# Kernel optimization log

Hardware: AMD Instinct MI355X
Metric: run time of the kernel (lower is better)

## Reference

```python
import jax, jax.numpy as jnp
import numpy as np

N, E, G = 100000, 300000, 4096
ND, ED, H, ZI, ZS, NE, L = 64, 16, 256, 128, 128, 8, 3
LAMBDA_GRL = 1.0


def setup_inputs() -> dict:
    key = jax.random.key(0)
    ks = iter(jax.random.split(key, 64))
    def nrm(shape, scale=0.05):
        return jax.random.normal(next(ks), shape, jnp.float32) * scale
    inp = {
        'x': jax.random.normal(next(ks), (N, ND), jnp.float32),
        'edge_index': jax.random.randint(next(ks), (2, E), 0, N),
        'edge_attr': jax.random.normal(next(ks), (E, ED), jnp.float32),
        'batch': jnp.sort(jax.random.randint(next(ks), (N,), 0, G)),
        'node_W': nrm((ND, H)), 'node_b': nrm((H,)),
        'conv_eps': jnp.zeros((L,), jnp.float32),
        'edge_W': nrm((L, ED, H)), 'edge_b': nrm((L, H)),
        'mlp_W1': nrm((L, H, H)), 'mlp_b1': nrm((L, H)),
        'mlp_W2': nrm((L, H, H)), 'mlp_b2': nrm((L, H)),
        'gn_w': jnp.ones((L, H), jnp.float32), 'gn_b': jnp.zeros((L, H), jnp.float32),
        'gn_ms': jnp.ones((L, H), jnp.float32),
        'finv_W1': nrm((H, ZI)), 'finv_b1': nrm((ZI,)),
        'finv_W2': nrm((ZI, ZI)), 'finv_b2': nrm((ZI,)),
        'fspu_W1': nrm((H, ZS)), 'fspu_b1': nrm((ZS,)),
        'fspu_W2': nrm((ZS, ZS)), 'fspu_b2': nrm((ZS,)),
        'pred_W1': nrm((ZI, ZI)), 'pred_b1': nrm((ZI,)),
        'pred_W2': nrm((ZI, 1)), 'pred_b2': nrm((1,)),
        'adv_W1': nrm((ZI, ZI)), 'adv_b1': nrm((ZI,)),
        'adv_W2': nrm((ZI, NE)), 'adv_b2': nrm((NE,)),
    }
    return inp


def _mlp2(h, W1, b1, W2, b2):
    return jax.nn.relu(h @ W1 + b1) @ W2 + b2


def reference(x, edge_index, edge_attr, batch, node_W, node_b, conv_eps,
              edge_W, edge_b, mlp_W1, mlp_b1, mlp_W2, mlp_b2,
              gn_w, gn_b, gn_ms,
              finv_W1, finv_b1, finv_W2, finv_b2,
              fspu_W1, fspu_b1, fspu_W2, fspu_b2,
              pred_W1, pred_b1, pred_W2, pred_b2,
              adv_W1, adv_b1, adv_W2, adv_b2):
    src, dst = edge_index[0], edge_index[1]
    cnt = jax.ops.segment_sum(jnp.ones((N, 1), jnp.float32), batch, num_segments=G)
    cnt = jnp.maximum(cnt, 1.0)
    h = x @ node_W + node_b  # [N,H]
    for l in range(L):
        # GINEConv: sum_j relu(x_j + lin(e_ij))
        e = edge_attr @ edge_W[l] + edge_b[l]            # [E,H]
        m = jax.nn.relu(h[src] + e)                      # [E,H]
        agg = jax.ops.segment_sum(m, dst, num_segments=N)
        h = _mlp2((1.0 + conv_eps[l]) * h + agg, mlp_W1[l], mlp_b1[l], mlp_W2[l], mlp_b2[l])
        # GraphNorm
        mean = jax.ops.segment_sum(h, batch, num_segments=G) / cnt  # [G,H]
        out = h - gn_ms[l] * mean[batch]
        var = jax.ops.segment_sum(out * out, batch, num_segments=G) / cnt
        h = out * jax.lax.rsqrt(var[batch] + 1e-5) * gn_w[l] + gn_b[l]
        h = jax.nn.relu(h)  # dropout is identity at eval
    hg = jax.ops.segment_sum(h, batch, num_segments=G) / cnt  # global_mean_pool [G,H]
    z_inv = _mlp2(hg, finv_W1, finv_b1, finv_W2, finv_b2)
    z_spu = _mlp2(hg, fspu_W1, fspu_b1, fspu_W2, fspu_b2)
    yhat = _mlp2(z_inv, pred_W1, pred_b1, pred_W2, pred_b2)[:, 0]
    # gradient reversal: identity fwd, -lambda on bwd
    grl = jax.lax.stop_gradient(z_inv) * (1.0 + LAMBDA_GRL) - LAMBDA_GRL * z_inv
    envhat = _mlp2(grl, adv_W1, adv_b1, adv_W2, adv_b2)
    return (hg, z_inv, z_spu, yhat, envhat)
```

## Files before the change

kernel.cpp:

```cpp
#include <hip/hip_runtime.h>
#include <hip/hip_bf16.h>

typedef __bf16 bf16_t;
typedef __bf16 bf16x8 __attribute__((ext_vector_type(8)));
typedef __bf16 bf16x4 __attribute__((ext_vector_type(4)));
typedef float  f32x4  __attribute__((ext_vector_type(4)));

static constexpr int N_NODES = 100000;
static constexpr int N_EDGES = 300000;
static constexpr int N_GRAPH = 4096;
static constexpr int H  = 256;
static constexpr int ND = 64;
static constexpr int ZIC = 128;
static constexpr int NE = 8;
static constexpr int SCAN_B = 1024;

__device__ __forceinline__ int clampi(int v, int lo, int hi) {
  return v < lo ? lo : (v > hi ? hi : v);
}

__device__ __forceinline__ void dma16(const bf16_t* g, bf16_t* lds_base) {
  __builtin_amdgcn_global_load_lds(
      (const __attribute__((address_space(1))) void*)g,
      (__attribute__((address_space(3))) void*)lds_base, 16, 0, 0);
}

__global__ void compute_starts_kernel(const int* __restrict__ batch,
                                      int* __restrict__ starts,
                                      int* __restrict__ counts,
                                      int* __restrict__ cursor, int N, int G) {
  int i = blockIdx.x * blockDim.x + threadIdx.x;
  if (i >= N) return;
  counts[i] = 0;
  cursor[i] = 0;
  int b = clampi(batch[i], 0, G - 1);
  if (i == 0) {
    for (int g = 0; g <= b; ++g) starts[g] = 0;
  } else {
    int p = clampi(batch[i - 1], 0, G - 1);
    for (int g = p + 1; g <= b; ++g) starts[g] = i;
  }
  if (i == N - 1) {
    for (int g = b + 1; g <= G; ++g) starts[g] = N;
  }
}

__global__ void count_deg_kernel(const int* __restrict__ dst, int* __restrict__ counts, int E, int N) {
  int e = blockIdx.x * blockDim.x + threadIdx.x;
  if (e < E) atomicAdd(&counts[clampi(dst[e], 0, N - 1)], 1);
}

__global__ __launch_bounds__(SCAN_B) void scan1_kernel(const int* __restrict__ counts,
                                                       int* __restrict__ offs,
                                                       int* __restrict__ bsum, int N) {
  __shared__ int tmp[SCAN_B];
  int i = blockIdx.x * SCAN_B + threadIdx.x;
  int v = (i < N) ? counts[i] : 0;
  tmp[threadIdx.x] = v;
  __syncthreads();
  for (int d = 1; d < SCAN_B; d <<= 1) {
    int t = (threadIdx.x >= d) ? tmp[threadIdx.x - d] : 0;
    __syncthreads();
    tmp[threadIdx.x] += t;
    __syncthreads();
  }
  if (i < N) offs[i + 1] = tmp[threadIdx.x];
  if (threadIdx.x == SCAN_B - 1) bsum[blockIdx.x] = tmp[SCAN_B - 1];
  if (i == 0) offs[0] = 0;
}

__global__ void scan2_kernel(int* __restrict__ bsum, int nblk) {
  if (blockIdx.x == 0 && threadIdx.x == 0) {
    int run = 0;
    for (int b = 0; b < nblk; ++b) { int v = bsum[b]; bsum[b] = run; run += v; }
  }
}

__global__ __launch_bounds__(SCAN_B) void scan3_kernel(int* __restrict__ offs,
                                                       const int* __restrict__ bsum, int N) {
  int i = blockIdx.x * SCAN_B + threadIdx.x;
  if (i < N) offs[i + 1] += bsum[blockIdx.x];
}

__global__ void fill_scatter_kernel(const int* __restrict__ src, const int* __restrict__ dst,
                                    const float* __restrict__ eattr,
                                    const int* __restrict__ offs, int* __restrict__ cursor,
                                    int* __restrict__ src_srt, bf16_t* __restrict__ eat16,
                                    int E, int N) {
  int e = blockIdx.x * blockDim.x + threadIdx.x;
  if (e >= E) return;
  int d = clampi(dst[e], 0, N - 1);
  int pos = offs[d] + atomicAdd(&cursor[d], 1);
  if ((unsigned)pos >= (unsigned)E) return;
  int s = src[e];
  src_srt[pos] = ((unsigned)s < (unsigned)N_NODES) ? s : 0;
  const float* ea = eattr + (size_t)e * 16;
  union { bf16_t b[16]; uint4 u[2]; } pk;
#pragma unroll
  for (int k = 0; k < 16; ++k) pk.b[k] = (bf16_t)ea[k];
  uint4* dst16 = (uint4*)(eat16 + ((size_t)pos << 4));
  dst16[0] = pk.u[0];
  dst16[1] = pk.u[1];
}

__global__ void build_ewt16_kernel(const float* __restrict__ edge_W,
                                   bf16_t* __restrict__ ewt) {
  int idx = blockIdx.x * blockDim.x + threadIdx.x;
  if (idx >= 3 * 256 * 16) return;
  int l = idx / (256 * 16);
  int rem = idx - l * 256 * 16;
  int n = rem >> 4, k = rem & 15;
  ewt[idx] = (bf16_t)edge_W[(size_t)l * 16 * 256 + k * 256 + n];
}

__global__ void transpose_kernel(const float* __restrict__ W,
                                 bf16_t* __restrict__ Wt, int K, int Nc,
                                 size_t srcStride, size_t dstStride) {
  __shared__ float tile[32][33];
  const float* Wz = W + (size_t)blockIdx.z * srcStride;
  bf16_t* Wtz = Wt + (size_t)blockIdx.z * dstStride;
  int n0 = blockIdx.x * 32, k0 = blockIdx.y * 32;
  int tx = threadIdx.x, ty = threadIdx.y;
  for (int i = ty; i < 32; i += 8)
    tile[i][tx] = Wz[(size_t)(k0 + i) * Nc + n0 + tx];
  __syncthreads();
  for (int i = ty; i < 32; i += 8)
    Wtz[(size_t)(n0 + i) * K + k0 + tx] = (bf16_t)tile[tx][i];
}

__device__ __forceinline__ void load8_to_lds(const bf16_t* p, bool valid, uint4* dst) {
  uint4 v = make_uint4(0u, 0u, 0u, 0u);
  if (valid) v = *(const uint4*)p;
  *dst = v;
}
__device__ __forceinline__ void load8_to_lds(const float* p, bool valid, uint4* dst) {
  float4 f0 = make_float4(0.f, 0.f, 0.f, 0.f), f1 = f0;
  if (valid) { f0 = *(const float4*)p; f1 = *(const float4*)(p + 4); }
  union { bf16_t b[8]; uint4 u; } pk;
  pk.b[0] = (bf16_t)f0.x; pk.b[1] = (bf16_t)f0.y;
  pk.b[2] = (bf16_t)f0.z; pk.b[3] = (bf16_t)f0.w;
  pk.b[4] = (bf16_t)f1.x; pk.b[5] = (bf16_t)f1.y;
  pk.b[6] = (bf16_t)f1.z; pk.b[7] = (bf16_t)f1.w;
  *dst = pk.u;
}

template<int K, bool RELU, bool OUTF32, typename TIN>
__global__ __launch_bounds__(256) void gemm128_kernel(
    const TIN* __restrict__ U, const bf16_t* __restrict__ Wt,
    const float* __restrict__ bias, void* __restrict__ Out, int M, int Nc) {
  constexpr int LDT = 72;
  __shared__ bf16_t Ut[128 * LDT];
  __shared__ bf16_t Wl[128 * LDT];
  const int m0 = blockIdx.x * 128;
  const int n0 = blockIdx.y * 128;
  const int t = threadIdx.x;
  const int lane = t & 63;
  const int wave = t >> 6;
  const int wm = (wave >> 1) * 64;
  const int wn = (wave & 1) * 64;
  const int srow = t >> 1;
  const int sk = (t & 1) * 32;
  const int lr = lane & 15;
  const int lq = lane >> 4;
  const bool aok = (m0 + srow) < M;
  f32x4 acc[4][4] = {};

  for (int k0 = 0; k0 < K; k0 += 64) {
    const TIN* up = U + (size_t)(m0 + srow) * K + k0 + sk;
    const bf16_t* wp = Wt + (size_t)(n0 + srow) * K + k0 + sk;
#pragma unroll
    for (int q = 0; q < 4; ++q) {
      load8_to_lds(up + q * 8, aok, (uint4*)&Ut[srow * LDT + sk + q * 8]);
      load8_to_lds(wp + q * 8, true, (uint4*)&Wl[srow * LDT + sk + q * 8]);
    }
    __syncthreads();
#pragma unroll
    for (int s = 0; s < 2; ++s) {
      bf16x8 a[4], b[4];
#pragma unroll
      for (int mt = 0; mt < 4; ++mt)
        a[mt] = *(const bf16x8*)(&Ut[(wm + mt * 16 + lr) * LDT + s * 32 + lq * 8]);
#pragma unroll
      for (int nt = 0; nt < 4; ++nt)
        b[nt] = *(const bf16x8*)(&Wl[(wn + nt * 16 + lr) * LDT + s * 32 + lq * 8]);
#pragma unroll
      for (int mt = 0; mt < 4; ++mt)
#pragma unroll
        for (int nt = 0; nt < 4; ++nt)
          acc[mt][nt] = __builtin_amdgcn_mfma_f32_16x16x32_bf16(
              a[mt], b[nt], acc[mt][nt], 0, 0, 0);
    }
    __syncthreads();
  }

#pragma unroll
  for (int mt = 0; mt < 4; ++mt)
#pragma unroll
    for (int nt = 0; nt < 4; ++nt) {
      int col = n0 + wn + nt * 16 + lr;
      float bcol = bias[col];
#pragma unroll
      for (int r = 0; r < 4; ++r) {
        int row = m0 + wm + mt * 16 + lq * 4 + r;
        if (row < M) {
          float vv = acc[mt][nt][r] + bcol;
          if (RELU) vv = vv > 0.f ? vv : 0.f;
          if (OUTF32) ((float*)Out)[(size_t)row * Nc + col] = vv;
          else        ((bf16_t*)Out)[(size_t)row * Nc + col] = (bf16_t)vv;
        }
      }
    }
}

template<int K, bool RELU, bool OUTF32, typename TIN>
__global__ __launch_bounds__(256) void gemm64x2_kernel(
    const TIN* __restrict__ U0, const bf16_t* __restrict__ Wt0,
    const float* __restrict__ b0, void* __restrict__ O0,
    const TIN* __restrict__ U1, const bf16_t* __restrict__ Wt1,
    const float* __restrict__ b1, void* __restrict__ O1, int M, int Nc) {
  constexpr int LDT = 72;
  __shared__ bf16_t Ut[64 * LDT];
  __shared__ bf16_t Wl[64 * LDT];
  const TIN*    U    = blockIdx.z ? U1 : U0;
  const bf16_t* Wt   = blockIdx.z ? Wt1 : Wt0;
  const float*  bias = blockIdx.z ? b1 : b0;
  void*         Out  = blockIdx.z ? O1 : O0;
  const int m0 = blockIdx.x * 64;
  const int n0 = blockIdx.y * 64;
  const int t = threadIdx.x;
  const int lane = t & 63;
  const int wave = t >> 6;
  const int wm = (wave >> 1) * 32;
  const int wn = (wave & 1) * 32;
  const int srow = t >> 2;
  const int sk = (t & 3) * 8;
  const int lr = lane & 15;
  const int lq = lane >> 4;
  const bool aok = (m0 + srow) < M;
  f32x4 acc[2][2] = {};

  for (int k0 = 0; k0 < K; k0 += 64) {
    const TIN* up = U + (size_t)(m0 + srow) * K + k0 + sk;
    const bf16_t* wp = Wt + (size_t)(n0 + srow) * K + k0 + sk;
    load8_to_lds(up,      aok, (uint4*)&Ut[srow * LDT + sk]);
    load8_to_lds(up + 32, aok, (uint4*)&Ut[srow * LDT + sk + 32]);
    load8_to_lds(wp,      true, (uint4*)&Wl[srow * LDT + sk]);
    load8_to_lds(wp + 32, true, (uint4*)&Wl[srow * LDT + sk + 32]);
    __syncthreads();
#pragma unroll
    for (int s = 0; s < 2; ++s) {
      bf16x8 a[2], b[2];
#pragma unroll
      for (int mt = 0; mt < 2; ++mt)
        a[mt] = *(const bf16x8*)(&Ut[(wm + mt * 16 + lr) * LDT + s * 32 + lq * 8]);
#pragma unroll
      for (int nt = 0; nt < 2; ++nt)
        b[nt] = *(const bf16x8*)(&Wl[(wn + nt * 16 + lr) * LDT + s * 32 + lq * 8]);
#pragma unroll
      for (int mt = 0; mt < 2; ++mt)
#pragma unroll
        for (int nt = 0; nt < 2; ++nt)
          acc[mt][nt] = __builtin_amdgcn_mfma_f32_16x16x32_bf16(
              a[mt], b[nt], acc[mt][nt], 0, 0, 0);
    }
    __syncthreads();
  }

#pragma unroll
  for (int mt = 0; mt < 2; ++mt)
#pragma unroll
    for (int nt = 0; nt < 2; ++nt) {
      int col = n0 + wn + nt * 16 + lr;
      float bcol = bias[col];
#pragma unroll
      for (int r = 0; r < 4; ++r) {
        int row = m0 + wm + mt * 16 + lq * 4 + r;
        if (row < M) {
          float vv = acc[mt][nt][r] + bcol;
          if (RELU) vv = vv > 0.f ? vv : 0.f;
          if (OUTF32) ((float*)Out)[(size_t)row * Nc + col] = vv;
          else        ((bf16_t*)Out)[(size_t)row * Nc + col] = (bf16_t)vv;
        }
      }
    }
}

template<int K, bool RELU>
__global__ __launch_bounds__(512) void gemm256_dma_kernel(
    const bf16_t* __restrict__ U, const bf16_t* __restrict__ Wt,
    const float* __restrict__ bias, bf16_t* __restrict__ Out, int M) {
  __shared__ bf16_t Ut[128 * 64];
  __shared__ bf16_t Wl[256 * 64];
  const int t = threadIdx.x;
  const int lane = t & 63;
  const int wave = t >> 6;
  const int m0 = blockIdx.x * 128;
  const int wm = (wave >> 2) * 64;
  const int wn = (wave & 3) * 64;
  const int lr = lane & 15;
  const int lq = lane >> 4;
  const int subrow = lane >> 3;
  const int lchunk = (lane & 7) ^ subrow;
  f32x4 acc[4][4] = {};

  for (int k0 = 0; k0 < K; k0 += 64) {
#pragma unroll
    for (int c = 0; c < 2; ++c) {
      int urow = m0 + c * 64 + wave * 8 + subrow;
      if (urow >= M) urow = M - 1;
      dma16(U + (size_t)urow * K + k0 + lchunk * 8, &Ut[(c * 64 + wave * 8) * 64]);
    }
#pragma unroll
    for (int c = 0; c < 4; ++c) {
      int wrow = c * 64 + wave * 8 + subrow;
      dma16(Wt + (size_t)wrow * K + k0 + lchunk * 8, &Wl[(c * 64 + wave * 8) * 64]);
    }
    __syncthreads();
#pragma unroll
    for (int s = 0; s < 2; ++s) {
      bf16x8 a[4], b[4];
#pragma unroll
      for (int mt = 0; mt < 4; ++mt)
        a[mt] = *(const bf16x8*)(&Ut[(wm + mt * 16 + lr) * 64 + (((s * 4 + lq) ^ (lr & 7)) << 3)]);
#pragma unroll
      for (int nt = 0; nt < 4; ++nt)
        b[nt] = *(const bf16x8*)(&Wl[(wn + nt * 16 + lr) * 64 + (((s * 4 + lq) ^ (lr & 7)) << 3)]);
#pragma unroll
      for (int mt = 0; mt < 4; ++mt)
#pragma unroll
        for (int nt = 0; nt < 4; ++nt)
          acc[mt][nt] = __builtin_amdgcn_mfma_f32_16x16x32_bf16(
              a[mt], b[nt], acc[mt][nt], 0, 0, 0);
    }
    __syncthreads();
  }

#pragma unroll
  for (int mt = 0; mt < 4; ++mt)
#pragma unroll
    for (int nt = 0; nt < 4; ++nt) {
      int col = wn + nt * 16 + lr;
      float bcol = bias[col];
#pragma unroll
      for (int r = 0; r < 4; ++r) {
        int row = m0 + wm + mt * 16 + lq * 4 + r;
        if (row < M) {
          float vv = acc[mt][nt][r] + bcol;
          if (RELU) vv = vv > 0.f ? vv : 0.f;
          Out[(size_t)row * H + col] = (bf16_t)vv;
        }
      }
    }
}

__global__ __launch_bounds__(256) void gine_gather_mfma_kernel(
    const bf16_t* __restrict__ h, const bf16_t* __restrict__ eat16,
    const int* __restrict__ src_sorted, const int* __restrict__ offs,
    const bf16_t* __restrict__ ewt, const float* __restrict__ eb,
    const float* __restrict__ eps_p, bf16_t* __restrict__ u) {
  constexpr int HP = H + 8;
  __shared__ bf16_t slin[2][16 * HP];
  const int t = threadIdx.x;
  const int wave = t >> 6;
  const int lane = t & 63;
  const int lr = lane & 15;
  const int lq = lane >> 4;
  const int lane4 = lane * 4;
  const int n0 = blockIdx.x * 4;
  const int nodeN = n0 + wave;

  bf16x4 hs = *(const bf16x4*)(h + (size_t)nodeN * H + lane4);

  bf16x8 bfrag[4];
#pragma unroll
  for (int nt = 0; nt < 4; ++nt) {
    bf16x8 bv = {};
    if (lq < 2)
      bv = *(const bf16x8*)(ewt + ((wave * 64 + nt * 16 + lr) << 4) + (lq << 3));
    bfrag[nt] = bv;
  }
  float ebv[4];
#pragma unroll
  for (int i = 0; i < 4; ++i) ebv[i] = eb[lane4 + i];

  int bs = offs[n0], be = offs[n0 + 4];
  bs = clampi(bs, 0, N_EDGES);
  be = clampi(be, bs, N_EDGES);
  int ns = offs[nodeN], ne = offs[nodeN + 1];
  ns = clampi(ns, bs, be);
  ne = clampi(ne, ns, be);

  float acc[4] = {0.f, 0.f, 0.f, 0.f};
  int parity = 0;

  for (int cb = bs; cb < be; cb += 16, parity ^= 1) {
    int arow = cb + lr;
    if (arow >= N_EDGES) arow = N_EDGES - 1;
    bf16x8 afrag = {};
    if (lq < 2)
      afrag = *(const bf16x8*)(eat16 + ((size_t)arow << 4) + (lq << 3));

    int j0 = ns > cb ? ns : cb;
    int j1 = ne < cb + 16 ? ne : cb + 16;
    int sidx[4];
    bf16x4 hv[4];
    if (j0 < j1) {
#pragma unroll
      for (int q = 0; q < 4; ++q) {
        int jj = j0 + q; if (jj > j1 - 1) jj = j1 - 1;
        sidx[q] = src_sorted[jj];
      }
    }

    f32x4 c[4];
#pragma unroll
    for (int nt = 0; nt < 4; ++nt) {
      f32x4 z = {};
      c[nt] = __builtin_amdgcn_mfma_f32_16x16x32_bf16(afrag, bfrag[nt], z, 0, 0, 0);
    }
#pragma unroll
    for (int nt = 0; nt < 4; ++nt)
#pragma unroll
      for (int r = 0; r < 4; ++r)
        slin[parity][(lq * 4 + r) * HP + wave * 64 + nt * 16 + lr] = (bf16_t)c[nt][r];

    if (j0 < j1) {
#pragma unroll
      for (int q = 0; q < 4; ++q)
        hv[q] = *(const bf16x4*)(h + (size_t)sidx[q] * H + lane4);
    }

    __syncthreads();

    for (int jb = j0; jb < j1; jb += 4) {
      if (jb != j0) {
#pragma unroll
        for (int q = 0; q < 4; ++q) {
          int jj = jb + q; if (jj > j1 - 1) jj = j1 - 1;
          sidx[q] = src_sorted[jj];
        }
#pragma unroll
        for (int q = 0; q < 4; ++q)
          hv[q] = *(const bf16x4*)(h + (size_t)sidx[q] * H + lane4);
      }
#pragma unroll
      for (int q = 0; q < 4; ++q) {
        if (jb + q < j1) {
          bf16x4 lv = *(const bf16x4*)(&slin[parity][(jb + q - cb) * HP + lane4]);
#pragma unroll
          for (int i = 0; i < 4; ++i)
            acc[i] += fmaxf((float)hv[q][i] + (float)lv[i] + ebv[i], 0.f);
        }
      }
    }
  }

  const float sc = 1.0f + eps_p[0];
  union { bf16x4 v; uint2 b; } o;
#pragma unroll
  for (int i = 0; i < 4; ++i) o.v[i] = (bf16_t)(sc * (float)hs[i] + acc[i]);
  *(uint2*)(u + (size_t)nodeN * H + lane4) = o.b;
}

__global__ __launch_bounds__(256) void graphnorm_kernel(
    const bf16_t* __restrict__ v, bf16_t* __restrict__ hout,
    const int* __restrict__ starts,
    const float* __restrict__ w, const float* __restrict__ b,
    const float* __restrict__ ms, float* __restrict__ hg) {
  constexpr int RS = 9;
  constexpr int PS = 13;
  __shared__ float red[4 * 64 * RS];
  __shared__ float prm[64 * PS];
  const int g = blockIdx.x;
  const int t = threadIdx.x;
  const int lane = t & 63;
  const int wave = t >> 6;
  const int c0 = lane * 4;
  int s = starts[g], e = starts[g + 1];
  s = clampi(s, 0, N_NODES);
  e = clampi(e, s, N_NODES);
  const float cnt = (float)((e - s) > 1 ? (e - s) : 1);

  float sx[4] = {0.f, 0.f, 0.f, 0.f}, sxx[4] = {0.f, 0.f, 0.f, 0.f};
  {
    int i = s + wave;
    for (; i + 4 < e; i += 8) {
      bf16x4 x0 = *(const bf16x4*)(v + (size_t)i * H + c0);
      bf16x4 x1 = *(const bf16x4*)(v + (size_t)(i + 4) * H + c0);
#pragma unroll
      for (int j = 0; j < 4; ++j) {
        float f0 = (float)x0[j], f1 = (float)x1[j];
        sx[j] += f0 + f1; sxx[j] += f0 * f0 + f1 * f1;
      }
    }
    if (i < e) {
      bf16x4 x0 = *(const bf16x4*)(v + (size_t)i * H + c0);
#pragma unroll
      for (int j = 0; j < 4; ++j) {
        float f0 = (float)x0[j];
        sx[j] += f0; sxx[j] += f0 * f0;
      }
    }
  }
  float* myred = &red[(wave * 64 + lane) * RS];
#pragma unroll
  for (int j = 0; j < 4; ++j) { myred[j] = sx[j]; myred[4 + j] = sxx[j]; }
  __syncthreads();

  if (wave == 0) {
#pragma unroll
    for (int j = 0; j < 4; ++j) {
      float fsx = red[lane * RS + j] + red[(64 + lane) * RS + j] +
                  red[(128 + lane) * RS + j] + red[(192 + lane) * RS + j];
      float fsxx = red[lane * RS + 4 + j] + red[(64 + lane) * RS + 4 + j] +
                   red[(128 + lane) * RS + 4 + j] + red[(192 + lane) * RS + 4 + j];
      float mean = fsx / cnt;
      float sub = ms[c0 + j] * mean;
      float var = fsxx / cnt - 2.f * sub * mean + sub * sub;
      var = fmaxf(var, 0.f);
      prm[lane * PS + j] = sub;
      prm[lane * PS + 4 + j] = rsqrtf(var + 1e-5f) * w[c0 + j];
      prm[lane * PS + 8 + j] = b[c0 + j];
    }
  }
  __syncthreads();
  float sub[4], inv[4], bb[4];
#pragma unroll
  for (int j = 0; j < 4; ++j) {
    sub[j] = prm[lane * PS + j];
    inv[j] = prm[lane * PS + 4 + j];
    bb[j] = prm[lane * PS + 8 + j];
  }

  float psum[4] = {0.f, 0.f, 0.f, 0.f};
  {
    int i = s + wave;
    for (; i + 4 < e; i += 8) {
      bf16x4 x0 = *(const bf16x4*)(v + (size_t)i * H + c0);
      bf16x4 x1 = *(const bf16x4*)(v + (size_t)(i + 4) * H + c0);
      union { bf16x4 o; uint2 u; } p0, p1;
#pragma unroll
      for (int j = 0; j < 4; ++j) {
        float o0 = ((float)x0[j] - sub[j]) * inv[j] + bb[j];
        float o1 = ((float)x1[j] - sub[j]) * inv[j] + bb[j];
        o0 = o0 > 0.f ? o0 : 0.f;
        o1 = o1 > 0.f ? o1 : 0.f;
        psum[j] += o0 + o1;
        p0.o[j] = (bf16_t)o0; p1.o[j] = (bf16_t)o1;
      }
      *(uint2*)(hout + (size_t)i * H + c0) = p0.u;
      *(uint2*)(hout + (size_t)(i + 4) * H + c0) = p1.u;
    }
    if (i < e) {
      bf16x4 x0 = *(const bf16x4*)(v + (size_t)i * H + c0);
      union { bf16x4 o; uint2 u; } p0;
#pragma unroll
      for (int j = 0; j < 4; ++j) {
        float o0 = ((float)x0[j] - sub[j]) * inv[j] + bb[j];
        o0 = o0 > 0.f ? o0 : 0.f;
        psum[j] += o0;
        p0.o[j] = (bf16_t)o0;
      }
      *(uint2*)(hout + (size_t)i * H + c0) = p0.u;
    }
  }

  if (hg) {
#pragma unroll
    for (int j = 0; j < 4; ++j) myred[j] = psum[j];
    __syncthreads();
    if (wave == 0) {
#pragma unroll
      for (int j = 0; j < 4; ++j) {
        float p = red[lane * RS + j] + red[(64 + lane) * RS + j] +
                  red[(128 + lane) * RS + j] + red[(192 + lane) * RS + j];
        hg[(size_t)g * H + c0 + j] = p / cnt;
      }
    }
  }
}

__global__ void head_out2_kernel(const bf16_t* __restrict__ In1, const float* __restrict__ W1,
                                 const float* __restrict__ b1, float* __restrict__ O1,
                                 const bf16_t* __restrict__ In2, const float* __restrict__ W2,
                                 const float* __restrict__ b2, float* __restrict__ O2,
                                 int M) {
  int idx = blockIdx.x * blockDim.x + threadIdx.x;
  if (idx < M) {
    float acc = b1[0];
    const bf16_t* in = In1 + (size_t)idx * ZIC;
    for (int k = 0; k < ZIC; ++k) acc += (float)in[k] * W1[k];
    O1[idx] = acc;
  } else {
    int j = idx - M;
    if (j >= M * NE) return;
    int r = j >> 3, n = j & 7;
    float acc = b2[n];
    const bf16_t* in = In2 + (size_t)r * ZIC;
    for (int k = 0; k < ZIC; ++k) acc += (float)in[k] * W2[(size_t)k * NE + n];
    O2[j] = acc;
  }
}

extern "C" void kernel_launch(void* const* d_in, const int* in_sizes, int n_in,
                              void* d_out, int out_size, void* d_ws, size_t ws_size,
                              hipStream_t stream) {
  (void)in_sizes; (void)n_in; (void)out_size; (void)ws_size;
  const float* x        = (const float*)d_in[0];
  const int*   eidx     = (const int*)d_in[1];
  const float* eattr    = (const float*)d_in[2];
  const int*   batch    = (const int*)d_in[3];
  const float* node_W   = (const float*)d_in[4];
  const float* node_b   = (const float*)d_in[5];
  const float* conv_eps = (const float*)d_in[6];
  const float* edge_W   = (const float*)d_in[7];
  const float* edge_b   = (const float*)d_in[8];
  const float* mlp_W1   = (const float*)d_in[9];
  const float* mlp_b1   = (const float*)d_in[10];
  const float* mlp_W2   = (const float*)d_in[11];
  const float* mlp_b2   = (const float*)d_in[12];
  const float* gn_w     = (const float*)d_in[13];
  const float* gn_b     = (const float*)d_in[14];
  const float* gn_ms    = (const float*)d_in[15];
  const float* finv_W1  = (const float*)d_in[16];
  const float* finv_b1  = (const float*)d_in[17];
  const float* finv_W2  = (const float*)d_in[18];
  const float* finv_b2  = (const float*)d_in[19];
  const float* fspu_W1  = (const float*)d_in[20];
  const float* fspu_b1  = (const float*)d_in[21];
  const float* fspu_W2  = (const float*)d_in[22];
  const float* fspu_b2  = (const float*)d_in[23];
  const float* pred_W1  = (const float*)d_in[24];
  const float* pred_b1  = (const float*)d_in[25];
  const float* pred_W2  = (const float*)d_in[26];
  const float* pred_b2  = (const float*)d_in[27];
  const float* adv_W1   = (const float*)d_in[28];
  const float* adv_b1   = (const float*)d_in[29];
  const float* adv_W2   = (const float*)d_in[30];
  const float* adv_b2   = (const float*)d_in[31];
  float* out = (float*)d_out;

  float* out_hg = out;
  float* out_zi = out + (size_t)N_GRAPH * H;
  float* out_zs = out_zi + (size_t)N_GRAPH * ZIC;
  float* out_yh = out_zs + (size_t)N_GRAPH * ZIC;
  float* out_ev = out_yh + N_GRAPH;

  char* wp = (char*)d_ws;
  auto alloc = [&](size_t bytes) { char* p = wp; wp += (bytes + 255) & ~(size_t)255; return p; };
  bf16_t* A        = (bf16_t*)alloc((size_t)N_NODES * H * 2);
  bf16_t* B        = (bf16_t*)alloc((size_t)N_NODES * H * 2);
  bf16_t* Wt       = (bf16_t*)alloc((size_t)(H * ND + 6 * H * H) * 2);
  bf16_t* WtH      = (bf16_t*)alloc((size_t)(2 * ZIC * H + 4 * ZIC * ZIC) * 2);
  bf16_t* ewt16    = (bf16_t*)alloc((size_t)3 * 256 * 16 * 2);
  bf16_t* eat16    = (bf16_t*)alloc((size_t)N_EDGES * 16 * 2);
  int*    starts   = (int*)alloc((size_t)(N_GRAPH + 1) * 4);
  int*    counts   = (int*)alloc((size_t)N_NODES * 4);
  int*    cursor   = (int*)alloc((size_t)N_NODES * 4);
  int*    offs     = (int*)alloc((size_t)(N_NODES + 1) * 4);
  int*    bsum     = (int*)alloc((size_t)SCAN_B * 4);
  int*    src_srt  = (int*)alloc((size_t)N_EDGES * 4);
  bf16_t* tmp1     = (bf16_t*)alloc((size_t)N_GRAPH * ZIC * 2);
  bf16_t* tmp2     = (bf16_t*)alloc((size_t)N_GRAPH * ZIC * 2);

  const int* srcp = eidx;
  const int* dstp = eidx + N_EDGES;
  const int nscan = (N_NODES + SCAN_B - 1) / SCAN_B;

  compute_starts_kernel<<<(N_NODES + 255) / 256, 256, 0, stream>>>(
      batch, starts, counts, cursor, N_NODES, N_GRAPH);
  count_deg_kernel<<<(N_EDGES + 255) / 256, 256, 0, stream>>>(dstp, counts, N_EDGES, N_NODES);
  scan1_kernel<<<nscan, SCAN_B, 0, stream>>>(counts, offs, bsum, N_NODES);
  scan2_kernel<<<1, 64, 0, stream>>>(bsum, nscan);
  scan3_kernel<<<nscan, SCAN_B, 0, stream>>>(offs, bsum, N_NODES);
  fill_scatter_kernel<<<(N_EDGES + 255) / 256, 256, 0, stream>>>(
      srcp, dstp, eattr, offs, cursor, src_srt, eat16, N_EDGES, N_NODES);
  build_ewt16_kernel<<<(3 * 256 * 16 + 255) / 256, 256, 0, stream>>>(edge_W, ewt16);

  bf16_t* WtN = Wt;
  bf16_t* Wt1base = Wt + H * ND;
  bf16_t* Wt2base = Wt + H * ND + (size_t)H * H;
  auto Wt1l = [&](int l) { return Wt1base + (size_t)(2 * l) * H * H; };
  auto Wt2l = [&](int l) { return Wt2base + (size_t)(2 * l) * H * H; };
  transpose_kernel<<<dim3(H / 32, ND / 32, 1), dim3(32, 8), 0, stream>>>(node_W, WtN, ND, H, 0, 0);
  transpose_kernel<<<dim3(H / 32, H / 32, 3), dim3(32, 8), 0, stream>>>(
      mlp_W1, Wt1base, H, H, (size_t)H * H, (size_t)2 * H * H);
  transpose_kernel<<<dim3(H / 32, H / 32, 3), dim3(32, 8), 0, stream>>>(
      mlp_W2, Wt2base, H, H, (size_t)H * H, (size_t)2 * H * H);

  bf16_t* fT1 = WtH;
  bf16_t* fT2 = fT1 + ZIC * H;
  bf16_t* sT1 = fT2 + ZIC * ZIC;
  bf16_t* sT2 = sT1 + ZIC * H;
  bf16_t* pT1 = sT2 + ZIC * ZIC;
  bf16_t* aT1 = pT1 + ZIC * ZIC;
  transpose_kernel<<<dim3(ZIC / 32, H / 32, 1), dim3(32, 8), 0, stream>>>(finv_W1, fT1, H, ZIC, 0, 0);
  transpose_kernel<<<dim3(ZIC / 32, ZIC / 32, 1), dim3(32, 8), 0, stream>>>(finv_W2, fT2, ZIC, ZIC, 0, 0);
  transpose_kernel<<<dim3(ZIC / 32, H / 32, 1), dim3(32, 8), 0, stream>>>(fspu_W1, sT1, H, ZIC, 0, 0);
  transpose_kernel<<<dim3(ZIC / 32, ZIC / 32, 1), dim3(32, 8), 0, stream>>>(fspu_W2, sT2, ZIC, ZIC, 0, 0);
  transpose_kernel<<<dim3(ZIC / 32, ZIC / 32, 1), dim3(32, 8), 0, stream>>>(pred_W1, pT1, ZIC, ZIC, 0, 0);
  transpose_kernel<<<dim3(ZIC / 32, ZIC / 32, 1), dim3(32, 8), 0, stream>>>(adv_W1, aT1, ZIC, ZIC, 0, 0);

  dim3 ggrid((N_NODES + 127) / 128, H / 128);
  gemm128_kernel<ND, false, false><<<ggrid, 256, 0, stream>>>(x, WtN, node_b, A, N_NODES, H);

  const int mblocks = (N_NODES + 127) / 128;
  for (int l = 0; l < 3; ++l) {
    gine_gather_mfma_kernel<<<N_NODES / 4, 256, 0, stream>>>(
        A, eat16, src_srt, offs, ewt16 + (size_t)l * 256 * 16,
        edge_b + l * H, conv_eps + l, B);
    gemm256_dma_kernel<H, true ><<<mblocks, 512, 0, stream>>>(B, Wt1l(l), mlp_b1 + l * H, A, N_NODES);
    gemm256_dma_kernel<H, false><<<mblocks, 512, 0, stream>>>(A, Wt2l(l), mlp_b2 + l * H, B, N_NODES);
    graphnorm_kernel<<<N_GRAPH, 256, 0, stream>>>(B, A, starts, gn_w + l * H, gn_b + l * H,
                                                  gn_ms + l * H, (l == 2) ? out_hg : nullptr);
  }

  dim3 hgrid2(N_GRAPH / 64, ZIC / 64, 2);
  gemm64x2_kernel<H, true, false, float><<<hgrid2, 256, 0, stream>>>(
      out_hg, fT1, finv_b1, tmp1, out_hg, sT1, fspu_b1, tmp2, N_GRAPH, ZIC);
  gemm64x2_kernel<ZIC, false, true, bf16_t><<<hgrid2, 256, 0, stream>>>(
      tmp1, fT2, finv_b2, out_zi, tmp2, sT2, fspu_b2, out_zs, N_GRAPH, ZIC);
  gemm64x2_kernel<ZIC, true, false, float><<<hgrid2, 256, 0, stream>>>(
      out_zi, pT1, pred_b1, tmp1, out_zi, aT1, adv_b1, tmp2, N_GRAPH, ZIC);
  head_out2_kernel<<<(N_GRAPH * (1 + NE) + 255) / 256, 256, 0, stream>>>(
      tmp1, pred_W2, pred_b2, out_yh, tmp2, adv_W2, adv_b2, out_ev, N_GRAPH);
}
```

Measured before the change: 729.0 us.

## Fuse the two MLP GEMMs per layer, keeping the hidden activation in LDS

Replaces the two separate 256-wide GEMM launches of each GIN MLP with one kernel. It computes relu(U·W1+b1) into a swizzled 128x256 LDS tile and then multiplies that tile by W2. This removes the global write and re-read of the intermediate activation and one launch per layer. The W1 transpose gains a channel permutation so each lane's accumulator columns pack contiguously into LDS. Weight fragments are now loaded straight from global memory (L2) instead of being staged in LDS. The larger LDS footprint may also reduce occupancy.

```diff
diff --git a/kernel.cpp b/kernel.cpp
--- a/kernel.cpp
+++ b/kernel.cpp
@@ -126,6 +126,24 @@
   __syncthreads();
   for (int i = ty; i < 32; i += 8)
     Wtz[(size_t)(n0 + i) * K + k0 + tx] = (bf16_t)tile[tx][i];
+}
+
+__global__ void transpose_perm_kernel(const float* __restrict__ W,
+                                      bf16_t* __restrict__ Wt, int K,
+                                      size_t srcStride, size_t dstStride) {
+  __shared__ float tile[32][33];
+  const float* Wz = W + (size_t)blockIdx.z * srcStride;
+  bf16_t* Wtz = Wt + (size_t)blockIdx.z * dstStride;
+  int n0 = blockIdx.x * 32, k0 = blockIdx.y * 32;
+  int tx = threadIdx.x, ty = threadIdx.y;
+  for (int i = ty; i < 32; i += 8)
+    tile[i][tx] = Wz[(size_t)(k0 + i) * 256 + n0 + tx];
+  __syncthreads();
+  for (int i = ty; i < 32; i += 8) {
+    int n = n0 + i;
+    int s = ((n & 15) << 4) | (n >> 4);
+    Wtz[(size_t)s * K + k0 + tx] = (bf16_t)tile[tx][i];
+  }
 }
 
 __device__ __forceinline__ void load8_to_lds(const bf16_t* p, bool valid, uint4* dst) {
@@ -285,12 +303,13 @@
     }
 }
 
-template<int K, bool RELU>
-__global__ __launch_bounds__(512) void gemm256_dma_kernel(
-    const bf16_t* __restrict__ U, const bf16_t* __restrict__ Wt,
-    const float* __restrict__ bias, bf16_t* __restrict__ Out, int M) {
+template<int K>
+__global__ __launch_bounds__(512, 4) void mlp_fused_kernel(
+    const bf16_t* __restrict__ U, const bf16_t* __restrict__ W1p,
+    const float* __restrict__ b1, const bf16_t* __restrict__ W2t,
+    const float* __restrict__ b2, bf16_t* __restrict__ Out, int M) {
+  __shared__ bf16_t T[128 * 256];
   __shared__ bf16_t Ut[128 * 64];
-  __shared__ bf16_t Wl[256 * 64];
   const int t = threadIdx.x;
   const int lane = t & 63;
   const int wave = t >> 6;
@@ -310,21 +329,16 @@
       if (urow >= M) urow = M - 1;
       dma16(U + (size_t)urow * K + k0 + lchunk * 8, &Ut[(c * 64 + wave * 8) * 64]);
     }
-#pragma unroll
-    for (int c = 0; c < 4; ++c) {
-      int wrow = c * 64 + wave * 8 + subrow;
-      dma16(Wt + (size_t)wrow * K + k0 + lchunk * 8, &Wl[(c * 64 + wave * 8) * 64]);
-    }
     __syncthreads();
 #pragma unroll
     for (int s = 0; s < 2; ++s) {
       bf16x8 a[4], b[4];
 #pragma unroll
+      for (int nt = 0; nt < 4; ++nt)
+        b[nt] = *(const bf16x8*)(W1p + (size_t)(wn + nt * 16 + lr) * K + k0 + s * 32 + lq * 8);
+#pragma unroll
       for (int mt = 0; mt < 4; ++mt)
         a[mt] = *(const bf16x8*)(&Ut[(wm + mt * 16 + lr) * 64 + (((s * 4 + lq) ^ (lr & 7)) << 3)]);
-#pragma unroll
-      for (int nt = 0; nt < 4; ++nt)
-        b[nt] = *(const bf16x8*)(&Wl[(wn + nt * 16 + lr) * 64 + (((s * 4 + lq) ^ (lr & 7)) << 3)]);
 #pragma unroll
       for (int mt = 0; mt < 4; ++mt)
 #pragma unroll
@@ -335,18 +349,64 @@
     __syncthreads();
   }
 
+  {
+    const int ch0 = lr * 16 + (wave & 3) * 4;
+    float b1v[4];
+#pragma unroll
+    for (int nt = 0; nt < 4; ++nt) b1v[nt] = b1[ch0 + nt];
+#pragma unroll
+    for (int mt = 0; mt < 4; ++mt)
+#pragma unroll
+      for (int r = 0; r < 4; ++r) {
+        int row = wm + mt * 16 + lq * 4 + r;
+        union { bf16_t b[4]; uint2 u2; } pk;
+#pragma unroll
+        for (int nt = 0; nt < 4; ++nt) {
+          float vv = acc[mt][nt][r] + b1v[nt];
+          pk.b[nt] = (bf16_t)(vv > 0.f ? vv : 0.f);
+        }
+        *(uint2*)((char*)T + (row << 9) + ((ch0 * 2) ^ ((row & 7) << 4))) = pk.u2;
+      }
+  }
+  __syncthreads();
+
+#pragma unroll
+  for (int mt = 0; mt < 4; ++mt)
+#pragma unroll
+    for (int nt = 0; nt < 4; ++nt) {
+      f32x4 z = {};
+      acc[mt][nt] = z;
+    }
+  for (int k2 = 0; k2 < K; k2 += 32) {
+    bf16x8 a[4], b[4];
+#pragma unroll
+    for (int nt = 0; nt < 4; ++nt)
+      b[nt] = *(const bf16x8*)(W2t + (size_t)(wn + nt * 16 + lr) * K + k2 + lq * 8);
+#pragma unroll
+    for (int mt = 0; mt < 4; ++mt) {
+      int row = wm + mt * 16 + lr;
+      a[mt] = *(const bf16x8*)((const char*)T + (row << 9) +
+                               (((k2 + lq * 8) * 2) ^ ((row & 7) << 4)));
+    }
+#pragma unroll
+    for (int mt = 0; mt < 4; ++mt)
+#pragma unroll
+      for (int nt = 0; nt < 4; ++nt)
+        acc[mt][nt] = __builtin_amdgcn_mfma_f32_16x16x32_bf16(
+            a[mt], b[nt], acc[mt][nt], 0, 0, 0);
+  }
+
 #pragma unroll
   for (int mt = 0; mt < 4; ++mt)
 #pragma unroll
     for (int nt = 0; nt < 4; ++nt) {
       int col = wn + nt * 16 + lr;
-      float bcol = bias[col];
+      float bcol = b2[col];
 #pragma unroll
       for (int r = 0; r < 4; ++r) {
         int row = m0 + wm + mt * 16 + lq * 4 + r;
         if (row < M) {
           float vv = acc[mt][nt][r] + bcol;
-          if (RELU) vv = vv > 0.f ? vv : 0.f;
           Out[(size_t)row * H + col] = (bf16_t)vv;
         }
       }
@@ -683,8 +743,8 @@
   auto Wt1l = [&](int l) { return Wt1base + (size_t)(2 * l) * H * H; };
   auto Wt2l = [&](int l) { return Wt2base + (size_t)(2 * l) * H * H; };
   transpose_kernel<<<dim3(H / 32, ND / 32, 1), dim3(32, 8), 0, stream>>>(node_W, WtN, ND, H, 0, 0);
-  transpose_kernel<<<dim3(H / 32, H / 32, 3), dim3(32, 8), 0, stream>>>(
-      mlp_W1, Wt1base, H, H, (size_t)H * H, (size_t)2 * H * H);
+  transpose_perm_kernel<<<dim3(H / 32, H / 32, 3), dim3(32, 8), 0, stream>>>(
+      mlp_W1, Wt1base, H, (size_t)H * H, (size_t)2 * H * H);
   transpose_kernel<<<dim3(H / 32, H / 32, 3), dim3(32, 8), 0, stream>>>(
       mlp_W2, Wt2base, H, H, (size_t)H * H, (size_t)2 * H * H);
 
@@ -709,8 +769,8 @@
     gine_gather_mfma_kernel<<<N_NODES / 4, 256, 0, stream>>>(
         A, eat16, src_srt, offs, ewt16 + (size_t)l * 256 * 16,
         edge_b + l * H, conv_eps + l, B);
-    gemm256_dma_kernel<H, true ><<<mblocks, 512, 0, stream>>>(B, Wt1l(l), mlp_b1 + l * H, A, N_NODES);
-    gemm256_dma_kernel<H, false><<<mblocks, 512, 0, stream>>>(A, Wt2l(l), mlp_b2 + l * H, B, N_NODES);
+    mlp_fused_kernel<H><<<mblocks, 512, 0, stream>>>(
+        B, Wt1l(l), mlp_b1 + l * H, Wt2l(l), mlp_b2 + l * H, B, N_NODES);
     graphnorm_kernel<<<N_GRAPH, 256, 0, stream>>>(B, A, starts, gn_w + l * H, gn_b + l * H,
                                                   gn_ms + l * H, (l == 2) ? out_hg : nullptr);
   }
```

Measured after the change: 755.6 us. +3.6%, slower.

## Fuse all prediction-head MLP layers into one kernel with LDS intermediates

Applied to the files above, without the earlier changes.

Replaces the three two-way GEMM launches and the final output kernel with a single kernel. Each block processes 64 graphs through the finv/fspu MLPs, the pred/adv first layers and the final projections, keeping intermediates in shared memory. This removes launch overhead and global round-trips of temporary buffers, but uses only 64 blocks and reads weight operands directly from global memory.

```diff
diff --git a/kernel.cpp b/kernel.cpp
--- a/kernel.cpp
+++ b/kernel.cpp
@@ -212,79 +212,6 @@
     }
 }
 
-template<int K, bool RELU, bool OUTF32, typename TIN>
-__global__ __launch_bounds__(256) void gemm64x2_kernel(
-    const TIN* __restrict__ U0, const bf16_t* __restrict__ Wt0,
-    const float* __restrict__ b0, void* __restrict__ O0,
-    const TIN* __restrict__ U1, const bf16_t* __restrict__ Wt1,
-    const float* __restrict__ b1, void* __restrict__ O1, int M, int Nc) {
-  constexpr int LDT = 72;
-  __shared__ bf16_t Ut[64 * LDT];
-  __shared__ bf16_t Wl[64 * LDT];
-  const TIN*    U    = blockIdx.z ? U1 : U0;
-  const bf16_t* Wt   = blockIdx.z ? Wt1 : Wt0;
-  const float*  bias = blockIdx.z ? b1 : b0;
-  void*         Out  = blockIdx.z ? O1 : O0;
-  const int m0 = blockIdx.x * 64;
-  const int n0 = blockIdx.y * 64;
-  const int t = threadIdx.x;
-  const int lane = t & 63;
-  const int wave = t >> 6;
-  const int wm = (wave >> 1) * 32;
-  const int wn = (wave & 1) * 32;
-  const int srow = t >> 2;
-  const int sk = (t & 3) * 8;
-  const int lr = lane & 15;
-  const int lq = lane >> 4;
-  const bool aok = (m0 + srow) < M;
-  f32x4 acc[2][2] = {};
-
-  for (int k0 = 0; k0 < K; k0 += 64) {
-    const TIN* up = U + (size_t)(m0 + srow) * K + k0 + sk;
-    const bf16_t* wp = Wt + (size_t)(n0 + srow) * K + k0 + sk;
-    load8_to_lds(up,      aok, (uint4*)&Ut[srow * LDT + sk]);
-    load8_to_lds(up + 32, aok, (uint4*)&Ut[srow * LDT + sk + 32]);
-    load8_to_lds(wp,      true, (uint4*)&Wl[srow * LDT + sk]);
-    load8_to_lds(wp + 32, true, (uint4*)&Wl[srow * LDT + sk + 32]);
-    __syncthreads();
-#pragma unroll
-    for (int s = 0; s < 2; ++s) {
-      bf16x8 a[2], b[2];
-#pragma unroll
-      for (int mt = 0; mt < 2; ++mt)
-        a[mt] = *(const bf16x8*)(&Ut[(wm + mt * 16 + lr) * LDT + s * 32 + lq * 8]);
-#pragma unroll
-      for (int nt = 0; nt < 2; ++nt)
-        b[nt] = *(const bf16x8*)(&Wl[(wn + nt * 16 + lr) * LDT + s * 32 + lq * 8]);
-#pragma unroll
-      for (int mt = 0; mt < 2; ++mt)
-#pragma unroll
-        for (int nt = 0; nt < 2; ++nt)
-          acc[mt][nt] = __builtin_amdgcn_mfma_f32_16x16x32_bf16(
-              a[mt], b[nt], acc[mt][nt], 0, 0, 0);
-    }
-    __syncthreads();
-  }
-
-#pragma unroll
-  for (int mt = 0; mt < 2; ++mt)
-#pragma unroll
-    for (int nt = 0; nt < 2; ++nt) {
-      int col = n0 + wn + nt * 16 + lr;
-      float bcol = bias[col];
-#pragma unroll
-      for (int r = 0; r < 4; ++r) {
-        int row = m0 + wm + mt * 16 + lq * 4 + r;
-        if (row < M) {
-          float vv = acc[mt][nt][r] + bcol;
-          if (RELU) vv = vv > 0.f ? vv : 0.f;
-          if (OUTF32) ((float*)Out)[(size_t)row * Nc + col] = vv;
-          else        ((bf16_t*)Out)[(size_t)row * Nc + col] = (bf16_t)vv;
-        }
-      }
-    }
-}
-
 template<int K, bool RELU>
 __global__ __launch_bounds__(512) void gemm256_dma_kernel(
     const bf16_t* __restrict__ U, const bf16_t* __restrict__ Wt,
@@ -580,25 +507,178 @@
   }
 }
 
-__global__ void head_out2_kernel(const bf16_t* __restrict__ In1, const float* __restrict__ W1,
-                                 const float* __restrict__ b1, float* __restrict__ O1,
-                                 const bf16_t* __restrict__ In2, const float* __restrict__ W2,
-                                 const float* __restrict__ b2, float* __restrict__ O2,
-                                 int M) {
-  int idx = blockIdx.x * blockDim.x + threadIdx.x;
-  if (idx < M) {
-    float acc = b1[0];
-    const bf16_t* in = In1 + (size_t)idx * ZIC;
-    for (int k = 0; k < ZIC; ++k) acc += (float)in[k] * W1[k];
-    O1[idx] = acc;
-  } else {
-    int j = idx - M;
-    if (j >= M * NE) return;
+__global__ __launch_bounds__(256) void heads_fused_kernel(
+    const float* __restrict__ hg,
+    const bf16_t* __restrict__ fT1, const float* __restrict__ fb1,
+    const bf16_t* __restrict__ fT2, const float* __restrict__ fb2,
+    const bf16_t* __restrict__ sT1, const float* __restrict__ sb1,
+    const bf16_t* __restrict__ sT2, const float* __restrict__ sb2,
+    const bf16_t* __restrict__ pT1, const float* __restrict__ pb1,
+    const bf16_t* __restrict__ aT1, const float* __restrict__ ab1,
+    const float* __restrict__ pW2, const float* __restrict__ pb2,
+    const float* __restrict__ aW2, const float* __restrict__ ab2,
+    float* __restrict__ out_zi, float* __restrict__ out_zs,
+    float* __restrict__ out_yh, float* __restrict__ out_ev) {
+  constexpr int LDS_S = 264;
+  constexpr int LDZ = 136;
+  __shared__ bf16_t BufA[64 * LDS_S];
+  __shared__ bf16_t BufB[64 * LDS_S];
+  __shared__ bf16_t Z[64 * LDZ];
+  const int t = threadIdx.x;
+  const int lane = t & 63;
+  const int wave = t >> 6;
+  const int m0 = blockIdx.x * 64;
+  const int lr = lane & 15;
+  const int lq = lane >> 4;
+
+  {
+    int r = t >> 2, cb = (t & 3) * 64;
+    const float* src = hg + (size_t)(m0 + r) * H + cb;
+#pragma unroll
+    for (int q = 0; q < 8; ++q)
+      load8_to_lds(src + q * 8, true, (uint4*)&BufA[r * LDS_S + cb + q * 8]);
+  }
+  __syncthreads();
+
+  f32x4 acc[4][4];
+
+  {
+    const bf16_t* W = (wave < 2) ? fT1 : sT1;
+    const float* bb = (wave < 2) ? fb1 : sb1;
+    const int wnl = (wave & 1) * 64;
+    const int wcol = wave * 64;
+#pragma unroll
+    for (int mt = 0; mt < 4; ++mt)
+#pragma unroll
+      for (int nt = 0; nt < 4; ++nt) { f32x4 z = {}; acc[mt][nt] = z; }
+    for (int k0 = 0; k0 < 256; k0 += 32) {
+      bf16x8 a[4], b[4];
+#pragma unroll
+      for (int nt = 0; nt < 4; ++nt)
+        b[nt] = *(const bf16x8*)(W + (size_t)(wnl + nt * 16 + lr) * 256 + k0 + lq * 8);
+#pragma unroll
+      for (int mt = 0; mt < 4; ++mt)
+        a[mt] = *(const bf16x8*)(&BufA[(mt * 16 + lr) * LDS_S + k0 + lq * 8]);
+#pragma unroll
+      for (int mt = 0; mt < 4; ++mt)
+#pragma unroll
+        for (int nt = 0; nt < 4; ++nt)
+          acc[mt][nt] = __builtin_amdgcn_mfma_f32_16x16x32_bf16(
+              a[mt], b[nt], acc[mt][nt], 0, 0, 0);
+    }
+    __syncthreads();
+#pragma unroll
+    for (int nt = 0; nt < 4; ++nt) {
+      float bv = bb[wnl + nt * 16 + lr];
+      int col = wcol + nt * 16 + lr;
+#pragma unroll
+      for (int mt = 0; mt < 4; ++mt)
+#pragma unroll
+        for (int r = 0; r < 4; ++r) {
+          int row = mt * 16 + lq * 4 + r;
+          float vv = acc[mt][nt][r] + bv;
+          BufB[row * LDS_S + col] = (bf16_t)(vv > 0.f ? vv : 0.f);
+        }
+    }
+  }
+  __syncthreads();
+
+  {
+    const bf16_t* W = (wave < 2) ? fT2 : sT2;
+    const float* bb = (wave < 2) ? fb2 : sb2;
+    float* outp = (wave < 2) ? out_zi : out_zs;
+    const int wnl = (wave & 1) * 64;
+    const int kin = (wave < 2) ? 0 : 128;
+#pragma unroll
+    for (int mt = 0; mt < 4; ++mt)
+#pragma unroll
+      for (int nt = 0; nt < 4; ++nt) { f32x4 z = {}; acc[mt][nt] = z; }
+    for (int k0 = 0; k0 < 128; k0 += 32) {
+      bf16x8 a[4], b[4];
+#pragma unroll
+      for (int nt = 0; nt < 4; ++nt)
+        b[nt] = *(const bf16x8*)(W + (size_t)(wnl + nt * 16 + lr) * 128 + k0 + lq * 8);
+#pragma unroll
+      for (int mt = 0; mt < 4; ++mt)
+        a[mt] = *(const bf16x8*)(&BufB[(mt * 16 + lr) * LDS_S + kin + k0 + lq * 8]);
+#pragma unroll
+      for (int mt = 0; mt < 4; ++mt)
+#pragma unroll
+        for (int nt = 0; nt < 4; ++nt)
+          acc[mt][nt] = __builtin_amdgcn_mfma_f32_16x16x32_bf16(
+              a[mt], b[nt], acc[mt][nt], 0, 0, 0);
+    }
+#pragma unroll
+    for (int nt = 0; nt < 4; ++nt) {
+      int col = wnl + nt * 16 + lr;
+      float bv = bb[col];
+#pragma unroll
+      for (int mt = 0; mt < 4; ++mt)
+#pragma unroll
+        for (int r = 0; r < 4; ++r) {
+          int row = mt * 16 + lq * 4 + r;
+          float vv = acc[mt][nt][r] + bv;
+          outp[(size_t)(m0 + row) * ZIC + col] = vv;
+          if (wave < 2) Z[row * LDZ + col] = (bf16_t)vv;
+        }
+    }
+  }
+  __syncthreads();
+
+  {
+    const bf16_t* W = (wave < 2) ? pT1 : aT1;
+    const float* bb = (wave < 2) ? pb1 : ab1;
+    const int wnl = (wave & 1) * 64;
+    const int wcol = wave * 64;
+#pragma unroll
+    for (int mt = 0; mt < 4; ++mt)
+#pragma unroll
+      for (int nt = 0; nt < 4; ++nt) { f32x4 z = {}; acc[mt][nt] = z; }
+    for (int k0 = 0; k0 < 128; k0 += 32) {
+      bf16x8 a[4], b[4];
+#pragma unroll
+      for (int nt = 0; nt < 4; ++nt)
+        b[nt] = *(const bf16x8*)(W + (size_t)(wnl + nt * 16 + lr) * 128 + k0 + lq * 8);
+#pragma unroll
+      for (int mt = 0; mt < 4; ++mt)
+        a[mt] = *(const bf16x8*)(&Z[(mt * 16 + lr) * LDZ + k0 + lq * 8]);
+#pragma unroll
+      for (int mt = 0; mt < 4; ++mt)
+#pragma unroll
+        for (int nt = 0; nt < 4; ++nt)
+          acc[mt][nt] = __builtin_amdgcn_mfma_f32_16x16x32_bf16(
+              a[mt], b[nt], acc[mt][nt], 0, 0, 0);
+    }
+#pragma unroll
+    for (int nt = 0; nt < 4; ++nt) {
+      float bv = bb[wnl + nt * 16 + lr];
+      int col = wcol + nt * 16 + lr;
+#pragma unroll
+      for (int mt = 0; mt < 4; ++mt)
+#pragma unroll
+        for (int r = 0; r < 4; ++r) {
+          int row = mt * 16 + lq * 4 + r;
+          float vv = acc[mt][nt][r] + bv;
+          BufA[row * LDS_S + col] = (bf16_t)(vv > 0.f ? vv : 0.f);
+        }
+    }
+  }
+  __syncthreads();
+
+  if (t < 64) {
+    float a4 = pb2[0];
+    for (int k = 0; k < 128; ++k)
+      a4 += (float)BufA[t * LDS_S + k] * pW2[k];
+    out_yh[m0 + t] = a4;
+  }
+#pragma unroll
+  for (int pass = 0; pass < 2; ++pass) {
+    int j = pass * 256 + t;
     int r = j >> 3, n = j & 7;
-    float acc = b2[n];
-    const bf16_t* in = In2 + (size_t)r * ZIC;
-    for (int k = 0; k < ZIC; ++k) acc += (float)in[k] * W2[(size_t)k * NE + n];
-    O2[j] = acc;
+    float a4 = ab2[n];
+    for (int k = 0; k < 128; ++k)
+      a4 += (float)BufA[r * LDS_S + 128 + k] * aW2[k * 8 + n];
+    out_ev[(size_t)(m0 + r) * NE + n] = a4;
   }
 }
 
@@ -660,8 +740,6 @@
   int*    offs     = (int*)alloc((size_t)(N_NODES + 1) * 4);
   int*    bsum     = (int*)alloc((size_t)SCAN_B * 4);
   int*    src_srt  = (int*)alloc((size_t)N_EDGES * 4);
-  bf16_t* tmp1     = (bf16_t*)alloc((size_t)N_GRAPH * ZIC * 2);
-  bf16_t* tmp2     = (bf16_t*)alloc((size_t)N_GRAPH * ZIC * 2);
 
   const int* srcp = eidx;
   const int* dstp = eidx + N_EDGES;
@@ -715,13 +793,11 @@
                                                   gn_ms + l * H, (l == 2) ? out_hg : nullptr);
   }
 
-  dim3 hgrid2(N_GRAPH / 64, ZIC / 64, 2);
-  gemm64x2_kernel<H, true, false, float><<<hgrid2, 256, 0, stream>>>(
-      out_hg, fT1, finv_b1, tmp1, out_hg, sT1, fspu_b1, tmp2, N_GRAPH, ZIC);
-  gemm64x2_kernel<ZIC, false, true, bf16_t><<<hgrid2, 256, 0, stream>>>(
-      tmp1, fT2, finv_b2, out_zi, tmp2, sT2, fspu_b2, out_zs, N_GRAPH, ZIC);
-  gemm64x2_kernel<ZIC, true, false, float><<<hgrid2, 256, 0, stream>>>(
-      out_zi, pT1, pred_b1, tmp1, out_zi, aT1, adv_b1, tmp2, N_GRAPH, ZIC);
-  head_out2_kernel<<<(N_GRAPH * (1 + NE) + 255) / 256, 256, 0, stream>>>(
-      tmp1, pred_W2, pred_b2, out_yh, tmp2, adv_W2, adv_b2, out_ev, N_GRAPH);
-}
+  heads_fused_kernel<<<N_GRAPH / 64, 256, 0, stream>>>(
+      out_hg,
+      fT1, finv_b1, fT2, finv_b2,
+      sT1, fspu_b1, sT2, fspu_b2,
+      pT1, pred_b1, aT1, adv_b1,
+      pred_W2, pred_b2, adv_W2, adv_b2,
+      out_zi, out_zs, out_yh, out_ev);
+}
```

New measurement: 722.5 us. Within noise of the previous version (-0.9%).
